# Kernel tuning notes

Measured on AMD Instinct MI355X. Metric: run time of the kernel, lower is better.

Reference implementation:

```python
import jax, jax.numpy as jnp
import numpy as np

N = 100000   # nodes
E = 1600000  # edges (avg degree 16)
F_IN = 128   # input node features
H = 8        # heads (layer 1)
F = 16       # features per head
C = 40       # num classes (layer 2, heads=1)
NEG_SLOPE = 0.2


def setup_inputs() -> dict:
    key = jax.random.key(0)
    ks = jax.random.split(key, 10)
    x = jax.random.normal(ks[0], (N, F_IN), dtype=jnp.float32)
    edge_src = jax.random.randint(ks[1], (E,), 0, N, dtype=jnp.int64)
    edge_dst = jax.random.randint(ks[2], (E,), 0, N, dtype=jnp.int64)
    # layer 1: F_IN -> H*F (concat heads)
    W1 = jax.random.normal(ks[3], (F_IN, H * F), dtype=jnp.float32) / np.sqrt(F_IN)
    att_src1 = jax.random.normal(ks[4], (H, F), dtype=jnp.float32) / np.sqrt(F)
    att_dst1 = jax.random.normal(ks[5], (H, F), dtype=jnp.float32) / np.sqrt(F)
    b1 = jnp.zeros((H * F,), dtype=jnp.float32)  # bias_init=zeros_
    # layer 2: H*F -> C with a single head
    W2 = jax.random.normal(ks[6], (H * F, C), dtype=jnp.float32) / np.sqrt(H * F)
    att_src2 = jax.random.normal(ks[7], (1, C), dtype=jnp.float32) / np.sqrt(C)
    att_dst2 = jax.random.normal(ks[8], (1, C), dtype=jnp.float32) / np.sqrt(C)
    b2 = jnp.zeros((C,), dtype=jnp.float32)
    return {"x": x, "edge_src": edge_src, "edge_dst": edge_dst,
            "W1": W1, "att_src1": att_src1, "att_dst1": att_dst1, "b1": b1,
            "W2": W2, "att_src2": att_src2, "att_dst2": att_dst2, "b2": b2}


def gat_conv(x, src, dst, W, a_src, a_dst, b, num_nodes):
    # PyG GATConv with add_self_loops=False, concat=True.
    nh, fh = a_src.shape
    h = (x @ W).reshape(-1, nh, fh)                      # [N, H, F]
    alpha_s = jnp.einsum('nhf,hf->nh', h, a_src)         # [N, H]
    alpha_d = jnp.einsum('nhf,hf->nh', h, a_dst)
    e = jax.nn.leaky_relu(alpha_s[src] + alpha_d[dst], NEG_SLOPE)  # [E, H]
    # segment softmax over incoming edges of each destination node
    m = jax.ops.segment_max(e, dst, num_segments=num_nodes)
    m = jnp.where(jnp.isfinite(m), m, 0.0)               # nodes w/o in-edges
    p = jnp.exp(e - m[dst])
    s = jax.ops.segment_sum(p, dst, num_segments=num_nodes)
    alpha = p / jnp.maximum(s[dst], 1e-16)               # [E, H]
    out = jax.ops.segment_sum(alpha[:, :, None] * h[src], dst,
                              num_segments=num_nodes)    # [N, H, F]
    return out.reshape(num_nodes, nh * fh) + b


def reference(x, edge_src, edge_dst, W1, att_src1, att_dst1, b1,
              W2, att_src2, att_dst2, b2):
    h = gat_conv(x, edge_src, edge_dst, W1, att_src1, att_dst1, b1, N)
    h = jax.nn.elu(h)
    return gat_conv(h, edge_src, edge_dst, W2, att_src2, att_dst2, b2, N)
```

## Files before the change

### kernel.cpp

```cpp
#include <hip/hip_runtime.h>
#include <cstdint>
#include <cstddef>

#define NN 100000
#define NE 1600000
#define NH 8
#define NC 40
#define NBKT 391
#define CHUNK 8192
#define P2BLKS ((NE + CHUNK - 1) / CHUNK)
#define G1BLKS 1563
#define BCBLKS 256

typedef _Float16 f16;
typedef f16 f16x2 __attribute__((ext_vector_type(2)));
typedef f16 f16x4 __attribute__((ext_vector_type(4)));
typedef f16 f16x8 __attribute__((ext_vector_type(8)));
typedef float f32x4 __attribute__((ext_vector_type(4)));

static __device__ __forceinline__ float leaky02(float x) {
  return x >= 0.f ? x : 0.2f * x;
}

static __device__ __forceinline__ int edge_at(const void* p, int is32, int i) {
  return is32 ? ((const int*)p)[i] : (int)((const long long*)p)[i];
}

__global__ __launch_bounds__(512) void init_kernel(int* __restrict__ flag,
                                                   int* __restrict__ gbucket) {
  const int t = threadIdx.x;
  if (t == 511) *flag = 0;
  if (t < NBKT) gbucket[t] = 0;
}

__global__ __launch_bounds__(256) void prepdet_kernel(
    const float* __restrict__ W1, const float* __restrict__ att_src,
    const float* __restrict__ att_dst, const float* __restrict__ W2,
    const float* __restrict__ as2v, const float* __restrict__ ad2v,
    const int* __restrict__ esrc32, f16* __restrict__ W2p,
    float* __restrict__ w1b2, int* __restrict__ flag) {
  if (blockIdx.x == 0) {
    for (int i = threadIdx.x; i < 8192; i += 256) {
      const int e = i & 7, lane = (i >> 3) & 63, t = (i >> 9) & 3, s = (i >> 11) & 3;
      const int k = 32 * s + ((lane >> 4) << 3) + e;
      const int c = 16 * t + (lane & 15);
      float v = 0.f;
      if (c < 40) {
        v = W2[k * 40 + c];
      } else if (c == 40 || c == 41) {
        const float* a = (c == 40) ? as2v : ad2v;
        float sacc = 0.f;
#pragma unroll 8
        for (int j = 0; j < 40; ++j) sacc += W2[k * 40 + j] * a[j];
        v = sacc;
      }
      W2p[i] = (f16)v;
    }
  } else if (blockIdx.x == 1) {
    const int k = threadIdx.x;
    if (k < 128) {
#pragma unroll
      for (int col = 0; col < 16; ++col) {
        const int h = col & 7;
        const float* av = (col < 8) ? att_src : att_dst;
        float v = 0.f;
#pragma unroll
        for (int f = 0; f < 16; ++f)
          v += W1[k * 128 + h * 16 + f] * av[h * 16 + f];
        w1b2[k * 16 + col] = v;
      }
    }
  } else {
    const int i = (blockIdx.x - 2) * 256 + threadIdx.x;
    if (i < 1024) {
      if (esrc32[2 * i + 1] != 0) atomicExch(flag, 1);
    }
  }
}

__global__ __launch_bounds__(256) void g1bc_kernel(
    const float* __restrict__ x, const float* __restrict__ W1,
    const float* __restrict__ w1b2, f16* __restrict__ h1,
    float* __restrict__ as1, float* __restrict__ ad1,
    const void* __restrict__ edst, const int* __restrict__ flag,
    int* __restrict__ gbucket) {
  __shared__ f16 wp[16384];
  __shared__ f16 wp2[2048];
  __shared__ int hcnt[NBKT];
  const int t = threadIdx.x;
  if (blockIdx.x >= G1BLKS) {
    for (int i = t; i < NBKT; i += 256) hcnt[i] = 0;
    __syncthreads();
    const int is32 = *flag;
    const int bid = blockIdx.x - G1BLKS;
    int i = bid * 256 + t;
    const int st = BCBLKS * 256;
    for (; i < NE; i += st) atomicAdd(&hcnt[edge_at(edst, is32, i) >> 8], 1);
    __syncthreads();
    for (int b = t; b < NBKT; b += 256)
      if (hcnt[b]) atomicAdd(&gbucket[b], hcnt[b]);
    return;
  }
  for (int i = t; i < 16384; i += 256) {
    const int e = i & 7, ln = (i >> 3) & 63, ct = (i >> 9) & 7, kt = i >> 12;
    const int k = kt * 32 + ((ln >> 4) << 3) + e;
    const int c = ct * 16 + (ln & 15);
    wp[i] = (f16)W1[k * 128 + c];
  }
  for (int i = t; i < 2048; i += 256) {
    const int e = i & 7, ln = (i >> 3) & 63, kt = i >> 9;
    const int k = kt * 32 + ((ln >> 4) << 3) + e;
    const int col = ln & 15;
    wp2[i] = (f16)w1b2[k * 16 + col];
  }
  __syncthreads();
  const int lane = t & 63;
  const int rsub = lane & 15, kg = lane >> 4;
  const int wid = (blockIdx.x * 256 + t) >> 6;
  if (wid >= NN / 16) return;
  const int row0 = wid * 16;
  const float* ap = x + (size_t)(row0 + rsub) * 128 + kg * 8;
  f16x8 a[4];
#pragma unroll
  for (int kt = 0; kt < 4; ++kt) {
    float4 v0 = *(const float4*)(ap + kt * 32);
    float4 v1 = *(const float4*)(ap + kt * 32 + 4);
    f16x8 av = { (f16)v0.x, (f16)v0.y, (f16)v0.z, (f16)v0.w,
                 (f16)v1.x, (f16)v1.y, (f16)v1.z, (f16)v1.w };
    a[kt] = av;
  }
  const f16x8* bp = (const f16x8*)wp;
  const f16x8* bp2 = (const f16x8*)wp2;
  const f32x4 z4 = { 0.f, 0.f, 0.f, 0.f };
  f32x4 acc[8];
#pragma unroll
  for (int ct = 0; ct < 8; ++ct) acc[ct] = z4;
  f32x4 acc2 = z4;
#pragma unroll
  for (int kt = 0; kt < 4; ++kt) {
#pragma unroll
    for (int ct = 0; ct < 8; ++ct)
      acc[ct] = __builtin_amdgcn_mfma_f32_16x16x32_f16(
          a[kt], bp[(kt * 8 + ct) * 64 + lane], acc[ct], 0, 0, 0);
    acc2 = __builtin_amdgcn_mfma_f32_16x16x32_f16(
        a[kt], bp2[kt * 64 + lane], acc2, 0, 0, 0);
  }
  const int r0 = row0 + kg * 4;
#pragma unroll
  for (int ct = 0; ct < 8; ++ct) {
#pragma unroll
    for (int r = 0; r < 4; ++r)
      h1[(size_t)(r0 + r) * 128 + ct * 16 + rsub] = (f16)acc[ct][r];
  }
#pragma unroll
  for (int r = 0; r < 4; ++r) {
    if (rsub < 8) as1[(r0 + r) * 8 + rsub] = acc2[r];
    else          ad1[(r0 + r) * 8 + rsub - 8] = acc2[r];
  }
}

__global__ __launch_bounds__(512) void bucketscan_kernel(
    const int* __restrict__ gbucket, int* __restrict__ bb,
    int* __restrict__ bcur) {
  __shared__ int wsum[8];
  const int t = threadIdx.x;
  const int lane = t & 63, w = t >> 6;
  int v = (t < NBKT) ? gbucket[t] : 0;
  int sc = v;
#pragma unroll
  for (int off = 1; off < 64; off <<= 1) {
    int o = __shfl_up(sc, off);
    if (lane >= off) sc += o;
  }
  if (lane == 63) wsum[w] = sc;
  __syncthreads();
  if (t < 8) {
    int ws = wsum[t];
#pragma unroll
    for (int off = 1; off < 8; off <<= 1) {
      int o = __shfl_up(ws, off);
      if (t >= off) ws += o;
    }
    wsum[t] = ws;
  }
  __syncthreads();
  if (w > 0) sc += wsum[w - 1];
  if (t < NBKT) {
    int ex = sc - v;
    bb[t] = ex;
    bcur[t] = ex;
  }
  if (t == NBKT - 1) bb[NBKT] = sc;
}

__global__ __launch_bounds__(256) void partition_kernel(
    const void* __restrict__ src, const void* __restrict__ dst,
    const int* __restrict__ flag, int* __restrict__ bcur,
    unsigned int* __restrict__ bucketbuf) {
  __shared__ int h[NBKT];
  __shared__ int gb[NBKT];
  const int t = threadIdx.x;
  const int is32 = *flag;
  const int lo = blockIdx.x * CHUNK;
  const int hi = min(lo + CHUNK, NE);
  for (int i = t; i < NBKT; i += 256) h[i] = 0;
  __syncthreads();
  for (int i = lo + t; i < hi; i += 256)
    atomicAdd(&h[edge_at(dst, is32, i) >> 8], 1);
  __syncthreads();
  for (int b = t; b < NBKT; b += 256)
    gb[b] = h[b] ? atomicAdd(&bcur[b], h[b]) : 0;
  __syncthreads();
  for (int i = t; i < NBKT; i += 256) h[i] = 0;
  __syncthreads();
  for (int i = lo + t; i < hi; i += 256) {
    int d = edge_at(dst, is32, i);
    int b = d >> 8;
    int s = atomicAdd(&h[b], 1);
    bucketbuf[gb[b] + s] =
        ((unsigned)(d & 255) << 17) | (unsigned)edge_at(src, is32, i);
  }
}

__global__ __launch_bounds__(256) void build_kernel(
    const unsigned int* __restrict__ bucketbuf, const int* __restrict__ bb,
    int* __restrict__ rowptr, int* __restrict__ csr) {
  __shared__ int cnt[256];
  __shared__ int cur[256];
  __shared__ int wsum[4];
  const int k = blockIdx.x;
  const int t = threadIdx.x;
  const int node0 = k << 8;
  const int lo = bb[k], hi = bb[k + 1];
  cnt[t] = 0;
  __syncthreads();
  for (int i = lo + t; i < hi; i += 256)
    atomicAdd(&cnt[bucketbuf[i] >> 17], 1);
  __syncthreads();
  const int lane = t & 63, w = t >> 6;
  const int v = cnt[t];
  int sc = v;
#pragma unroll
  for (int off = 1; off < 64; off <<= 1) {
    int o = __shfl_up(sc, off);
    if (lane >= off) sc += o;
  }
  if (lane == 63) wsum[w] = sc;
  __syncthreads();
  if (t < 4) {
    int ws = wsum[t];
#pragma unroll
    for (int off = 1; off < 4; off <<= 1) {
      int o = __shfl_up(ws, off);
      if (t >= off) ws += o;
    }
    wsum[t] = ws;
  }
  __syncthreads();
  if (w > 0) sc += wsum[w - 1];
  const int ex = lo + sc - v;
  const int node = node0 + t;
  if (node < NN) rowptr[node] = ex;
  if (node == NN - 1) rowptr[NN] = NE;
  cur[t] = ex;
  __syncthreads();
  for (int i = lo + t; i < hi; i += 256) {
    unsigned e = bucketbuf[i];
    int pos = atomicAdd(&cur[e >> 17], 1);
    csr[pos] = (int)(e & 0x1FFFF);
  }
}

__global__ __launch_bounds__(256) void agg1_kernel(
    const f16* __restrict__ h1, const float* __restrict__ as1,
    const float* __restrict__ ad1, const int* __restrict__ rowptr,
    const int* __restrict__ csr, f16* __restrict__ g1) {
  const int wid = (blockIdx.x * 256 + threadIdx.x) >> 6;
  const int lane = threadIdx.x & 63;
  if (wid >= NN) return;
  const int lo = rowptr[wid], hi = rowptr[wid + 1];
  const int deg = hi - lo;
  const int j = lane >> 3, hd = lane & 7;
  const float advv = ad1[wid * 8 + hd];
  float lk0 = -3.4e38f, lk1 = -3.4e38f, lk2 = -3.4e38f, lk3 = -3.4e38f;
  int s0 = 0, s1 = 0, s2 = 0, s3 = 0;
  if (j < deg)      { s0 = csr[lo + j];      lk0 = leaky02(as1[(size_t)s0 * 8 + hd] + advv); }
  if (8 + j < deg)  { s1 = csr[lo + 8 + j];  lk1 = leaky02(as1[(size_t)s1 * 8 + hd] + advv); }
  if (16 + j < deg) { s2 = csr[lo + 16 + j]; lk2 = leaky02(as1[(size_t)s2 * 8 + hd] + advv); }
  if (24 + j < deg) { s3 = csr[lo + 24 + j]; lk3 = leaky02(as1[(size_t)s3 * 8 + hd] + advv); }
  float m = fmaxf(fmaxf(lk0, lk1), fmaxf(lk2, lk3));
  for (int base = 32; base < deg; base += 8) {
    int e = base + j;
    float xv = (e < deg) ? leaky02(as1[(size_t)csr[lo + e] * 8 + hd] + advv)
                         : -3.4e38f;
    m = fmaxf(m, xv);
  }
  m = fmaxf(m, __shfl_xor(m, 8));
  m = fmaxf(m, __shfl_xor(m, 16));
  m = fmaxf(m, __shfl_xor(m, 32));
  const int q = lane >> 4;
  const int part = lane & 15;
  float sum = 0.f;
  float acc[8];
#pragma unroll
  for (int i = 0; i < 8; ++i) acc[i] = 0.f;
  for (int base = 0; base < deg; base += 8) {
    int e = base + j;
    float p = 0.f;
    int s = 0;
    if (base == 0)       { s = s0; if (e < deg) p = __expf(lk0 - m); }
    else if (base == 8)  { s = s1; if (e < deg) p = __expf(lk1 - m); }
    else if (base == 16) { s = s2; if (e < deg) p = __expf(lk2 - m); }
    else if (base == 24) { s = s3; if (e < deg) p = __expf(lk3 - m); }
    else if (e < deg) {
      s = csr[lo + e];
      p = __expf(leaky02(as1[(size_t)s * 8 + hd] + advv) - m);
    }
    sum += p;
    int sja = __shfl(s, q * 8);
    float pja = __shfl(p, q * 8 + (part >> 1));
    int sjb = __shfl(s, (4 + q) * 8);
    float pjb = __shfl(p, (4 + q) * 8 + (part >> 1));
    f16x8 hva = *(const f16x8*)(h1 + (size_t)sja * 128 + part * 8);
    f16x8 hvb = *(const f16x8*)(h1 + (size_t)sjb * 128 + part * 8);
#pragma unroll
    for (int i = 0; i < 8; ++i) acc[i] += pja * (float)hva[i];
#pragma unroll
    for (int i = 0; i < 8; ++i) acc[i] += pjb * (float)hvb[i];
  }
  sum += __shfl_xor(sum, 8);
  sum += __shfl_xor(sum, 16);
  sum += __shfl_xor(sum, 32);
#pragma unroll
  for (int i = 0; i < 8; ++i) {
    acc[i] += __shfl_xor(acc[i], 16);
    acc[i] += __shfl_xor(acc[i], 32);
  }
  float sden = __shfl(sum, part >> 1);
  float inv = 1.f / fmaxf(sden, 1e-16f);
  if (lane < 16) {
    f16x8 ov;
#pragma unroll
    for (int i = 0; i < 8; ++i) {
      float v = acc[i] * inv;
      v = v > 0.f ? v : (__expf(v) - 1.f);
      ov[i] = (f16)v;
    }
    *(f16x8*)(g1 + (size_t)wid * 128 + part * 8) = ov;
  }
}

__global__ __launch_bounds__(256) void gemm2_kernel(
    const f16* __restrict__ g1, const f16* __restrict__ W2p,
    f16* __restrict__ h2, float* __restrict__ as2, float* __restrict__ ad2) {
  const int lane = threadIdx.x & 63;
  const int wid = (blockIdx.x * 256 + threadIdx.x) >> 6;
  if (wid >= NN / 16) return;
  const int row0 = wid * 16;
  const int rsub = lane & 15;
  const int kg = lane >> 4;
  const f16* ap = g1 + (size_t)(row0 + rsub) * 128 + kg * 8;
  f16x8 a0 = *(const f16x8*)(ap);
  f16x8 a1 = *(const f16x8*)(ap + 32);
  f16x8 a2 = *(const f16x8*)(ap + 64);
  f16x8 a3 = *(const f16x8*)(ap + 96);
  const f16x8* bp = (const f16x8*)W2p;
  f32x4 acc[3];
  const f32x4 z4 = { 0.f, 0.f, 0.f, 0.f };
#pragma unroll
  for (int t = 0; t < 3; ++t) acc[t] = z4;
#pragma unroll
  for (int t = 0; t < 3; ++t) {
    acc[t] = __builtin_amdgcn_mfma_f32_16x16x32_f16(a0, bp[(0 * 4 + t) * 64 + lane], acc[t], 0, 0, 0);
    acc[t] = __builtin_amdgcn_mfma_f32_16x16x32_f16(a1, bp[(1 * 4 + t) * 64 + lane], acc[t], 0, 0, 0);
    acc[t] = __builtin_amdgcn_mfma_f32_16x16x32_f16(a2, bp[(2 * 4 + t) * 64 + lane], acc[t], 0, 0, 0);
    acc[t] = __builtin_amdgcn_mfma_f32_16x16x32_f16(a3, bp[(3 * 4 + t) * 64 + lane], acc[t], 0, 0, 0);
  }
  const int r0 = row0 + kg * 4;
#pragma unroll
  for (int t = 0; t < 3; ++t) {
    const int col = t * 16 + rsub;
    if (col < 40) {
#pragma unroll
      for (int r = 0; r < 4; ++r)
        h2[(size_t)(r0 + r) * 40 + col] = (f16)acc[t][r];
    }
  }
  if (rsub == 8) {
#pragma unroll
    for (int r = 0; r < 4; ++r) as2[r0 + r] = acc[2][r];
  } else if (rsub == 9) {
#pragma unroll
    for (int r = 0; r < 4; ++r) ad2[r0 + r] = acc[2][r];
  }
}

__global__ __launch_bounds__(256) void agg2_kernel(
    const f16* __restrict__ h2, const float* __restrict__ as2,
    const float* __restrict__ ad2, const int* __restrict__ rowptr,
    const int* __restrict__ csr, const float* __restrict__ b2,
    float* __restrict__ out) {
  const int wid = (blockIdx.x * 256 + threadIdx.x) >> 6;
  const int lane = threadIdx.x & 63;
  if (wid >= NN) return;
  const int lo = rowptr[wid], hi = rowptr[wid + 1];
  const int deg = hi - lo;
  const float advv = ad2[wid];
  float lkc = -3.4e38f;
  int sc = 0;
  if (lane < deg) {
    sc = csr[lo + lane];
    lkc = leaky02(as2[sc] + advv);
  }
  float m = lkc;
  for (int base = 64; base < deg; base += 64) {
    int e = base + lane;
    float xv = (e < deg) ? leaky02(as2[csr[lo + e]] + advv) : -3.4e38f;
    m = fmaxf(m, xv);
  }
#pragma unroll
  for (int off = 32; off >= 1; off >>= 1) m = fmaxf(m, __shfl_xor(m, off));
  const int j8 = lane >> 3, part8 = lane & 7;
  const bool pvon = part8 < 5;
  float sum = 0.f;
  float acc[8];
#pragma unroll
  for (int i = 0; i < 8; ++i) acc[i] = 0.f;
  for (int base = 0; base < deg; base += 64) {
    int e = base + lane;
    float p = 0.f;
    int s = 0;
    if (base == 0) {
      s = sc;
      if (lane < deg) p = __expf(lkc - m);
    } else if (e < deg) {
      s = csr[lo + e];
      p = __expf(leaky02(as2[s] + advv) - m);
    }
    sum += p;
    const int ng = (min(64, deg - base) + 7) >> 3;
    int g = 0;
    for (; g + 1 < ng; g += 2) {
      int sl1 = g * 8 + j8, sl2 = (g + 1) * 8 + j8;
      int sj1 = __shfl(s, sl1);
      float pj1 = __shfl(p, sl1);
      int sj2 = __shfl(s, sl2);
      float pj2 = __shfl(p, sl2);
      if (pvon) {
        f16x8 hv1 = *(const f16x8*)(h2 + (size_t)sj1 * 40 + part8 * 8);
        f16x8 hv2 = *(const f16x8*)(h2 + (size_t)sj2 * 40 + part8 * 8);
#pragma unroll
        for (int i = 0; i < 8; ++i) acc[i] += pj1 * (float)hv1[i];
#pragma unroll
        for (int i = 0; i < 8; ++i) acc[i] += pj2 * (float)hv2[i];
      }
    }
    if (g < ng) {
      int sl = g * 8 + j8;
      int sj = __shfl(s, sl);
      float pj = __shfl(p, sl);
      if (pvon) {
        f16x8 hv = *(const f16x8*)(h2 + (size_t)sj * 40 + part8 * 8);
#pragma unroll
        for (int i = 0; i < 8; ++i) acc[i] += pj * (float)hv[i];
      }
    }
  }
#pragma unroll
  for (int off = 32; off >= 1; off >>= 1) sum += __shfl_xor(sum, off);
#pragma unroll
  for (int i = 0; i < 8; ++i) {
    acc[i] += __shfl_xor(acc[i], 8);
    acc[i] += __shfl_xor(acc[i], 16);
    acc[i] += __shfl_xor(acc[i], 32);
  }
  const float inv = 1.f / fmaxf(sum, 1e-16f);
  if (lane < 5) {
    float4 b0 = *(const float4*)(b2 + lane * 8);
    float4 b1 = *(const float4*)(b2 + lane * 8 + 4);
    float4 v0 = { acc[0] * inv + b0.x, acc[1] * inv + b0.y,
                  acc[2] * inv + b0.z, acc[3] * inv + b0.w };
    float4 v1 = { acc[4] * inv + b1.x, acc[5] * inv + b1.y,
                  acc[6] * inv + b1.z, acc[7] * inv + b1.w };
    *(float4*)(out + (size_t)wid * 40 + lane * 8) = v0;
    *(float4*)(out + (size_t)wid * 40 + lane * 8 + 4) = v1;
  }
}

extern "C" void kernel_launch(void* const* d_in, const int* in_sizes, int n_in,
                              void* d_out, int out_size, void* d_ws, size_t ws_size,
                              hipStream_t stream) {
  (void)in_sizes; (void)n_in; (void)out_size; (void)ws_size;
  const float* x = (const float*)d_in[0];
  const void* esrc = d_in[1];
  const void* edst = d_in[2];
  const float* W1 = (const float*)d_in[3];
  const float* att_s1 = (const float*)d_in[4];
  const float* att_d1 = (const float*)d_in[5];
  const float* W2 = (const float*)d_in[7];
  const float* att_s2 = (const float*)d_in[8];
  const float* att_d2 = (const float*)d_in[9];
  const float* b2 = (const float*)d_in[10];

  char* p = (char*)d_ws;
  auto alloc = [&](size_t bytes) {
    char* q = p;
    p += (bytes + 255) & ~(size_t)255;
    return q;
  };
  f16* h1 = (f16*)alloc((size_t)NN * 128 * 2);
  f16* g1 = (f16*)alloc((size_t)NN * 128 * 2);
  f16* h2 = (f16*)alloc((size_t)NN * 40 * 2);
  float* as1 = (float*)alloc((size_t)NN * 8 * 4);
  float* ad1 = (float*)alloc((size_t)NN * 8 * 4);
  float* as2 = (float*)alloc((size_t)NN * 4);
  float* ad2 = (float*)alloc((size_t)NN * 4);
  f16* W2p = (f16*)alloc((size_t)8192 * 2);
  float* w1b2 = (float*)alloc((size_t)128 * 16 * 4);
  int* rowptr = (int*)alloc((size_t)(NN + 1) * 4);
  int* csr = (int*)alloc((size_t)NE * 4);
  unsigned int* bucketbuf = (unsigned int*)alloc((size_t)NE * 4);
  int* gbucket = (int*)alloc((size_t)NBKT * 4);
  int* bb = (int*)alloc((size_t)(NBKT + 1) * 4);
  int* bcur = (int*)alloc((size_t)NBKT * 4);
  int* flag = (int*)alloc(256);

  init_kernel<<<1, 512, 0, stream>>>(flag, gbucket);
  prepdet_kernel<<<6, 256, 0, stream>>>(W1, att_s1, att_d1, W2, att_s2,
                                        att_d2, (const int*)esrc, W2p, w1b2,
                                        flag);
  g1bc_kernel<<<G1BLKS + BCBLKS, 256, 0, stream>>>(x, W1, w1b2, h1, as1, ad1,
                                                   edst, flag, gbucket);
  bucketscan_kernel<<<1, 512, 0, stream>>>(gbucket, bb, bcur);
  partition_kernel<<<P2BLKS, 256, 0, stream>>>(esrc, edst, flag, bcur, bucketbuf);
  build_kernel<<<NBKT, 256, 0, stream>>>(bucketbuf, bb, rowptr, csr);
  agg1_kernel<<<25000, 256, 0, stream>>>(h1, as1, ad1, rowptr, csr, g1);
  gemm2_kernel<<<1563, 256, 0, stream>>>(g1, W2p, h2, as2, ad2);
  agg2_kernel<<<25000, 256, 0, stream>>>(h2, as2, ad2, rowptr, csr, b2, (float*)d_out);
}
```

Measured before the change: 253.2 us.

## Fuse layer-1 aggregation with layer-2 GEMM via shared memory, merge init into prep

Layer-1 aggregation now handles 16 nodes per block (4 per wave), writes the ELU outputs into shared memory, and runs the layer-2 MFMA projection in the same block. This removes the g1 global round trip and one kernel launch. The init kernel is folded into prepdet, which now clears the bucket counters and sets the int64 flag through a shared-memory OR. The partition chunk size is also halved. The risks are that only 3 of 4 waves do the GEMM and each wave serialises 4 nodes, which lowers the parallelism available to hide gather latency.

Measured after the change: 245.3 us. -3.1%, faster.

```diff
diff --git a/kernel.cpp b/kernel.cpp
--- a/kernel.cpp
+++ b/kernel.cpp
@@ -7,7 +7,7 @@
 #define NH 8
 #define NC 40
 #define NBKT 391
-#define CHUNK 8192
+#define CHUNK 4096
 #define P2BLKS ((NE + CHUNK - 1) / CHUNK)
 #define G1BLKS 1563
 #define BCBLKS 256
@@ -26,19 +26,14 @@
   return is32 ? ((const int*)p)[i] : (int)((const long long*)p)[i];
 }
 
-__global__ __launch_bounds__(512) void init_kernel(int* __restrict__ flag,
-                                                   int* __restrict__ gbucket) {
-  const int t = threadIdx.x;
-  if (t == 511) *flag = 0;
-  if (t < NBKT) gbucket[t] = 0;
-}
-
 __global__ __launch_bounds__(256) void prepdet_kernel(
     const float* __restrict__ W1, const float* __restrict__ att_src,
     const float* __restrict__ att_dst, const float* __restrict__ W2,
     const float* __restrict__ as2v, const float* __restrict__ ad2v,
     const int* __restrict__ esrc32, f16* __restrict__ W2p,
-    float* __restrict__ w1b2, int* __restrict__ flag) {
+    float* __restrict__ w1b2, int* __restrict__ flag,
+    int* __restrict__ gbucket) {
+  __shared__ int lflag;
   if (blockIdx.x == 0) {
     for (int i = threadIdx.x; i < 8192; i += 256) {
       const int e = i & 7, lane = (i >> 3) & 63, t = (i >> 9) & 3, s = (i >> 11) & 3;
@@ -70,11 +65,15 @@
         w1b2[k * 16 + col] = v;
       }
     }
+  } else if (blockIdx.x == 2) {
+    if (threadIdx.x == 0) lflag = 0;
+    __syncthreads();
+    for (int i = threadIdx.x; i < 1024; i += 256)
+      if (esrc32[2 * i + 1] != 0) atomicOr(&lflag, 1);
+    __syncthreads();
+    if (threadIdx.x == 0) *flag = lflag;
   } else {
-    const int i = (blockIdx.x - 2) * 256 + threadIdx.x;
-    if (i < 1024) {
-      if (esrc32[2 * i + 1] != 0) atomicExch(flag, 1);
-    }
+    for (int i = threadIdx.x; i < NBKT; i += 256) gbucket[i] = 0;
   }
 }
 
@@ -271,127 +270,119 @@
   }
 }
 
-__global__ __launch_bounds__(256) void agg1_kernel(
+__global__ __launch_bounds__(256) void agg1g2_kernel(
     const f16* __restrict__ h1, const float* __restrict__ as1,
     const float* __restrict__ ad1, const int* __restrict__ rowptr,
-    const int* __restrict__ csr, f16* __restrict__ g1) {
-  const int wid = (blockIdx.x * 256 + threadIdx.x) >> 6;
-  const int lane = threadIdx.x & 63;
-  if (wid >= NN) return;
-  const int lo = rowptr[wid], hi = rowptr[wid + 1];
-  const int deg = hi - lo;
+    const int* __restrict__ csr, const f16* __restrict__ W2p,
+    f16* __restrict__ h2, float* __restrict__ as2, float* __restrict__ ad2) {
+  __shared__ f16 g1s[16 * 128];
+  const int t = threadIdx.x;
+  const int lane = t & 63;
+  const int w = t >> 6;
   const int j = lane >> 3, hd = lane & 7;
-  const float advv = ad1[wid * 8 + hd];
-  float lk0 = -3.4e38f, lk1 = -3.4e38f, lk2 = -3.4e38f, lk3 = -3.4e38f;
-  int s0 = 0, s1 = 0, s2 = 0, s3 = 0;
-  if (j < deg)      { s0 = csr[lo + j];      lk0 = leaky02(as1[(size_t)s0 * 8 + hd] + advv); }
-  if (8 + j < deg)  { s1 = csr[lo + 8 + j];  lk1 = leaky02(as1[(size_t)s1 * 8 + hd] + advv); }
-  if (16 + j < deg) { s2 = csr[lo + 16 + j]; lk2 = leaky02(as1[(size_t)s2 * 8 + hd] + advv); }
-  if (24 + j < deg) { s3 = csr[lo + 24 + j]; lk3 = leaky02(as1[(size_t)s3 * 8 + hd] + advv); }
-  float m = fmaxf(fmaxf(lk0, lk1), fmaxf(lk2, lk3));
-  for (int base = 32; base < deg; base += 8) {
-    int e = base + j;
-    float xv = (e < deg) ? leaky02(as1[(size_t)csr[lo + e] * 8 + hd] + advv)
-                         : -3.4e38f;
-    m = fmaxf(m, xv);
-  }
-  m = fmaxf(m, __shfl_xor(m, 8));
-  m = fmaxf(m, __shfl_xor(m, 16));
-  m = fmaxf(m, __shfl_xor(m, 32));
   const int q = lane >> 4;
   const int part = lane & 15;
-  float sum = 0.f;
-  float acc[8];
-#pragma unroll
-  for (int i = 0; i < 8; ++i) acc[i] = 0.f;
-  for (int base = 0; base < deg; base += 8) {
-    int e = base + j;
-    float p = 0.f;
-    int s = 0;
-    if (base == 0)       { s = s0; if (e < deg) p = __expf(lk0 - m); }
-    else if (base == 8)  { s = s1; if (e < deg) p = __expf(lk1 - m); }
-    else if (base == 16) { s = s2; if (e < deg) p = __expf(lk2 - m); }
-    else if (base == 24) { s = s3; if (e < deg) p = __expf(lk3 - m); }
-    else if (e < deg) {
-      s = csr[lo + e];
-      p = __expf(leaky02(as1[(size_t)s * 8 + hd] + advv) - m);
-    }
-    sum += p;
-    int sja = __shfl(s, q * 8);
-    float pja = __shfl(p, q * 8 + (part >> 1));
-    int sjb = __shfl(s, (4 + q) * 8);
-    float pjb = __shfl(p, (4 + q) * 8 + (part >> 1));
-    f16x8 hva = *(const f16x8*)(h1 + (size_t)sja * 128 + part * 8);
-    f16x8 hvb = *(const f16x8*)(h1 + (size_t)sjb * 128 + part * 8);
-#pragma unroll
-    for (int i = 0; i < 8; ++i) acc[i] += pja * (float)hva[i];
-#pragma unroll
-    for (int i = 0; i < 8; ++i) acc[i] += pjb * (float)hvb[i];
-  }
-  sum += __shfl_xor(sum, 8);
-  sum += __shfl_xor(sum, 16);
-  sum += __shfl_xor(sum, 32);
-#pragma unroll
-  for (int i = 0; i < 8; ++i) {
-    acc[i] += __shfl_xor(acc[i], 16);
-    acc[i] += __shfl_xor(acc[i], 32);
-  }
-  float sden = __shfl(sum, part >> 1);
-  float inv = 1.f / fmaxf(sden, 1e-16f);
-  if (lane < 16) {
-    f16x8 ov;
+  const int base_node = blockIdx.x * 16 + w * 4;
+  for (int ii = 0; ii < 4; ++ii) {
+    const int wid = base_node + ii;
+    const int lo = rowptr[wid], hi = rowptr[wid + 1];
+    const int deg = hi - lo;
+    const float advv = ad1[wid * 8 + hd];
+    float lk0 = -3.4e38f, lk1 = -3.4e38f, lk2 = -3.4e38f, lk3 = -3.4e38f;
+    int s0 = 0, s1 = 0, s2 = 0, s3 = 0;
+    if (j < deg)      { s0 = csr[lo + j];      lk0 = leaky02(as1[(size_t)s0 * 8 + hd] + advv); }
+    if (8 + j < deg)  { s1 = csr[lo + 8 + j];  lk1 = leaky02(as1[(size_t)s1 * 8 + hd] + advv); }
+    if (16 + j < deg) { s2 = csr[lo + 16 + j]; lk2 = leaky02(as1[(size_t)s2 * 8 + hd] + advv); }
+    if (24 + j < deg) { s3 = csr[lo + 24 + j]; lk3 = leaky02(as1[(size_t)s3 * 8 + hd] + advv); }
+    float m = fmaxf(fmaxf(lk0, lk1), fmaxf(lk2, lk3));
+    for (int base = 32; base < deg; base += 8) {
+      int e = base + j;
+      float xv = (e < deg) ? leaky02(as1[(size_t)csr[lo + e] * 8 + hd] + advv)
+                           : -3.4e38f;
+      m = fmaxf(m, xv);
+    }
+    m = fmaxf(m, __shfl_xor(m, 8));
+    m = fmaxf(m, __shfl_xor(m, 16));
+    m = fmaxf(m, __shfl_xor(m, 32));
+    float sum = 0.f;
+    float acc[8];
+#pragma unroll
+    for (int i = 0; i < 8; ++i) acc[i] = 0.f;
+    for (int base = 0; base < deg; base += 8) {
+      int e = base + j;
+      float p = 0.f;
+      int s = 0;
+      if (base == 0)       { s = s0; if (e < deg) p = __expf(lk0 - m); }
+      else if (base == 8)  { s = s1; if (e < deg) p = __expf(lk1 - m); }
+      else if (base == 16) { s = s2; if (e < deg) p = __expf(lk2 - m); }
+      else if (base == 24) { s = s3; if (e < deg) p = __expf(lk3 - m); }
+      else if (e < deg) {
+        s = csr[lo + e];
+        p = __expf(leaky02(as1[(size_t)s * 8 + hd] + advv) - m);
+      }
+      sum += p;
+      int sja = __shfl(s, q * 8);
+      float pja = __shfl(p, q * 8 + (part >> 1));
+      int sjb = __shfl(s, (4 + q) * 8);
+      float pjb = __shfl(p, (4 + q) * 8 + (part >> 1));
+      f16x8 hva = *(const f16x8*)(h1 + (size_t)sja * 128 + part * 8);
+      f16x8 hvb = *(const f16x8*)(h1 + (size_t)sjb * 128 + part * 8);
+#pragma unroll
+      for (int i = 0; i < 8; ++i) acc[i] += pja * (float)hva[i];
+#pragma unroll
+      for (int i = 0; i < 8; ++i) acc[i] += pjb * (float)hvb[i];
+    }
+    sum += __shfl_xor(sum, 8);
+    sum += __shfl_xor(sum, 16);
+    sum += __shfl_xor(sum, 32);
 #pragma unroll
     for (int i = 0; i < 8; ++i) {
-      float v = acc[i] * inv;
-      v = v > 0.f ? v : (__expf(v) - 1.f);
-      ov[i] = (f16)v;
-    }
-    *(f16x8*)(g1 + (size_t)wid * 128 + part * 8) = ov;
-  }
-}
-
-__global__ __launch_bounds__(256) void gemm2_kernel(
-    const f16* __restrict__ g1, const f16* __restrict__ W2p,
-    f16* __restrict__ h2, float* __restrict__ as2, float* __restrict__ ad2) {
-  const int lane = threadIdx.x & 63;
-  const int wid = (blockIdx.x * 256 + threadIdx.x) >> 6;
-  if (wid >= NN / 16) return;
-  const int row0 = wid * 16;
-  const int rsub = lane & 15;
-  const int kg = lane >> 4;
-  const f16* ap = g1 + (size_t)(row0 + rsub) * 128 + kg * 8;
-  f16x8 a0 = *(const f16x8*)(ap);
-  f16x8 a1 = *(const f16x8*)(ap + 32);
-  f16x8 a2 = *(const f16x8*)(ap + 64);
-  f16x8 a3 = *(const f16x8*)(ap + 96);
-  const f16x8* bp = (const f16x8*)W2p;
-  f32x4 acc[3];
-  const f32x4 z4 = { 0.f, 0.f, 0.f, 0.f };
-#pragma unroll
-  for (int t = 0; t < 3; ++t) acc[t] = z4;
-#pragma unroll
-  for (int t = 0; t < 3; ++t) {
-    acc[t] = __builtin_amdgcn_mfma_f32_16x16x32_f16(a0, bp[(0 * 4 + t) * 64 + lane], acc[t], 0, 0, 0);
-    acc[t] = __builtin_amdgcn_mfma_f32_16x16x32_f16(a1, bp[(1 * 4 + t) * 64 + lane], acc[t], 0, 0, 0);
-    acc[t] = __builtin_amdgcn_mfma_f32_16x16x32_f16(a2, bp[(2 * 4 + t) * 64 + lane], acc[t], 0, 0, 0);
-    acc[t] = __builtin_amdgcn_mfma_f32_16x16x32_f16(a3, bp[(3 * 4 + t) * 64 + lane], acc[t], 0, 0, 0);
-  }
-  const int r0 = row0 + kg * 4;
-#pragma unroll
-  for (int t = 0; t < 3; ++t) {
-    const int col = t * 16 + rsub;
+      acc[i] += __shfl_xor(acc[i], 16);
+      acc[i] += __shfl_xor(acc[i], 32);
+    }
+    float sden = __shfl(sum, part >> 1);
+    float inv = 1.f / fmaxf(sden, 1e-16f);
+    if (lane < 16) {
+      f16x8 ov;
+#pragma unroll
+      for (int i = 0; i < 8; ++i) {
+        float v = acc[i] * inv;
+        v = v > 0.f ? v : (__expf(v) - 1.f);
+        ov[i] = (f16)v;
+      }
+      *(f16x8*)&g1s[(w * 4 + ii) * 128 + part * 8] = ov;
+    }
+  }
+  __syncthreads();
+  if (w < 3) {
+    const int rsub = lane & 15, kg = lane >> 4;
+    const f16* ap = &g1s[rsub * 128 + kg * 8];
+    f16x8 a0 = *(const f16x8*)(ap);
+    f16x8 a1 = *(const f16x8*)(ap + 32);
+    f16x8 a2 = *(const f16x8*)(ap + 64);
+    f16x8 a3 = *(const f16x8*)(ap + 96);
+    const f16x8* bp = (const f16x8*)W2p;
+    f32x4 acc2 = { 0.f, 0.f, 0.f, 0.f };
+    acc2 = __builtin_amdgcn_mfma_f32_16x16x32_f16(a0, bp[(0 * 4 + w) * 64 + lane], acc2, 0, 0, 0);
+    acc2 = __builtin_amdgcn_mfma_f32_16x16x32_f16(a1, bp[(1 * 4 + w) * 64 + lane], acc2, 0, 0, 0);
+    acc2 = __builtin_amdgcn_mfma_f32_16x16x32_f16(a2, bp[(2 * 4 + w) * 64 + lane], acc2, 0, 0, 0);
+    acc2 = __builtin_amdgcn_mfma_f32_16x16x32_f16(a3, bp[(3 * 4 + w) * 64 + lane], acc2, 0, 0, 0);
+    const int r0 = blockIdx.x * 16 + kg * 4;
+    const int col = w * 16 + rsub;
     if (col < 40) {
 #pragma unroll
       for (int r = 0; r < 4; ++r)
-        h2[(size_t)(r0 + r) * 40 + col] = (f16)acc[t][r];
-    }
-  }
-  if (rsub == 8) {
-#pragma unroll
-    for (int r = 0; r < 4; ++r) as2[r0 + r] = acc[2][r];
-  } else if (rsub == 9) {
-#pragma unroll
-    for (int r = 0; r < 4; ++r) ad2[r0 + r] = acc[2][r];
+        h2[(size_t)(r0 + r) * 40 + col] = (f16)acc2[r];
+    }
+    if (w == 2) {
+      if (rsub == 8) {
+#pragma unroll
+        for (int r = 0; r < 4; ++r) as2[r0 + r] = acc2[r];
+      } else if (rsub == 9) {
+#pragma unroll
+        for (int r = 0; r < 4; ++r) ad2[r0 + r] = acc2[r];
+      }
+    }
   }
 }
 
@@ -509,7 +500,6 @@
     return q;
   };
   f16* h1 = (f16*)alloc((size_t)NN * 128 * 2);
-  f16* g1 = (f16*)alloc((size_t)NN * 128 * 2);
   f16* h2 = (f16*)alloc((size_t)NN * 40 * 2);
   float* as1 = (float*)alloc((size_t)NN * 8 * 4);
   float* ad1 = (float*)alloc((size_t)NN * 8 * 4);
@@ -525,16 +515,16 @@
   int* bcur = (int*)alloc((size_t)NBKT * 4);
   int* flag = (int*)alloc(256);
 
-  init_kernel<<<1, 512, 0, stream>>>(flag, gbucket);
-  prepdet_kernel<<<6, 256, 0, stream>>>(W1, att_s1, att_d1, W2, att_s2,
+  prepdet_kernel<<<4, 256, 0, stream>>>(W1, att_s1, att_d1, W2, att_s2,
                                         att_d2, (const int*)esrc, W2p, w1b2,
-                                        flag);
+                                        flag, gbucket);
   g1bc_kernel<<<G1BLKS + BCBLKS, 256, 0, stream>>>(x, W1, w1b2, h1, as1, ad1,
                                                    edst, flag, gbucket);
   bucketscan_kernel<<<1, 512, 0, stream>>>(gbucket, bb, bcur);
   partition_kernel<<<P2BLKS, 256, 0, stream>>>(esrc, edst, flag, bcur, bucketbuf);
   build_kernel<<<NBKT, 256, 0, stream>>>(bucketbuf, bb, rowptr, csr);
-  agg1_kernel<<<25000, 256, 0, stream>>>(h1, as1, ad1, rowptr, csr, g1);
-  gemm2_kernel<<<1563, 256, 0, stream>>>(g1, W2p, h2, as2, ad2);
-  agg2_kernel<<<25000, 256, 0, stream>>>(h2, as2, ad2, rowptr, csr, b2, (float*)d_out);
-}
+  agg1g2_kernel<<<6250, 256, 0, stream>>>(h1, as1, ad1, rowptr, csr, W2p,
+                                          h2, as2, ad2);
+  agg2_kernel<<<25000, 256, 0, stream>>>(h2, as2, ad2, rowptr, csr, b2,
+                                         (float*)d_out);
+}
```
